# Kernel tuning notes

Measured on AMD Instinct MI355X. Metric: run time of the kernel, lower is better.

The kernel has to match this reference:

```python
import jax, jax.numpy as jnp
import numpy as np

LN_EPS = 1e-12


def setup_inputs() -> dict:
    key = jax.random.key(0)
    ks = jax.random.split(key, 10)
    B, S, W, D, H = 16, 512, 5, 200, 768
    std = 0.02
    return {
        "layer_output": jax.random.normal(ks[0], (B, S, H), dtype=jnp.float32),
        "word_embeddings": jax.random.normal(ks[1], (B, S, W, D), dtype=jnp.float32),
        "word_mask": jax.random.randint(ks[2], (B, S, W), 0, 2, dtype=jnp.int64),
        "W1": jax.random.normal(ks[3], (D, H), dtype=jnp.float32) * std,
        "b1": jnp.zeros((H,), dtype=jnp.float32),
        "W2": jax.random.normal(ks[4], (H, H), dtype=jnp.float32) * std,
        "b2": jnp.zeros((H,), dtype=jnp.float32),
        "attn_W": jax.random.normal(ks[5], (H, H), dtype=jnp.float32) * std,
        "ln_gamma": jnp.ones((H,), dtype=jnp.float32),
        "ln_beta": jnp.zeros((H,), dtype=jnp.float32),
    }


def reference(layer_output, word_embeddings, word_mask, W1, b1, W2, b2, attn_W, ln_gamma, ln_beta):
    # word_transform: Linear -> Tanh -> Linear (dropout = identity in eval)
    we = jnp.tanh(jnp.einsum("bswd,dh->bswh", word_embeddings, W1) + b1)
    we = jnp.einsum("bswh,hk->bswk", we, W2) + b2  # [B,S,W,H]

    # bilinear word attention: (x @ attn_W) . word_outputs -> score over W
    q = jnp.einsum("bsh,hk->bsk", layer_output, attn_W)  # [B,S,H]
    alpha = jnp.einsum("bsk,bswk->bsw", q, we)            # [B,S,W]
    alpha = alpha + (1.0 - word_mask.astype(alpha.dtype)) * -10000.0
    alpha = jax.nn.softmax(alpha, axis=-1)

    # weighted sum over words + residual
    agg = jnp.einsum("bsw,bswh->bsh", alpha, we)
    h = layer_output + agg

    # LayerNorm (fuse_layer; dropout = identity in eval)
    mu = jnp.mean(h, axis=-1, keepdims=True)
    var = jnp.mean(jnp.square(h - mu), axis=-1, keepdims=True)
    return (h - mu) * jax.lax.rsqrt(var + LN_EPS) * ln_gamma + ln_beta
```

## Files before the change

### kernel.cpp

```cpp
#include <hip/hip_runtime.h>
#include <hip/hip_bf16.h>
#include <math.h>


typedef __attribute__((ext_vector_type(8))) short bf16x8;
typedef __attribute__((ext_vector_type(4))) float f32x4;

__device__ __forceinline__ unsigned short f2bf_bits(float f) {
    __hip_bfloat16 h = __float2bfloat16(f);
    return *reinterpret_cast<unsigned short*>(&h);
}
__device__ __forceinline__ float bf_bits2f(unsigned short u) {
    union { unsigned int i; float f; } v; v.i = ((unsigned int)u) << 16; return v.f;
}
__device__ __forceinline__ float tanh_fast(float x) {
    float xc = fminf(fmaxf(x, -9.f), 9.f);
    float t  = __expf(2.f * xc);
    return (t - 1.f) * __builtin_amdgcn_rcpf(t + 1.f);
}
__device__ __forceinline__ bf16x8 pack8(float4 a, float4 b) {
    union { bf16x8 v; unsigned short s[8]; } u;
    u.s[0]=f2bf_bits(a.x); u.s[1]=f2bf_bits(a.y); u.s[2]=f2bf_bits(a.z); u.s[3]=f2bf_bits(a.w);
    u.s[4]=f2bf_bits(b.x); u.s[5]=f2bf_bits(b.y); u.s[6]=f2bf_bits(b.z); u.s[7]=f2bf_bits(b.w);
    return u.v;
}

__device__ __forceinline__ void async_cp16(const void* g, void* lds) {
#if __has_builtin(__builtin_amdgcn_global_load_lds)
    auto gp = (const __attribute__((address_space(1))) unsigned int*)g;
    auto lp = (__attribute__((address_space(3))) unsigned int*)lds;
    __builtin_amdgcn_global_load_lds(gp, lp, 16, 0, 0);
#else
    *(uint4*)lds = *(const uint4*)g;
#endif
}

__device__ __forceinline__ void sched_fence()  { asm volatile("" ::: "memory"); }
__device__ __forceinline__ void wait8_barrier(){ asm volatile("s_waitcnt vmcnt(8)\ns_barrier" ::: "memory"); }
__device__ __forceinline__ void wait4_barrier(){ asm volatile("s_waitcnt vmcnt(4)\ns_barrier" ::: "memory"); }
__device__ __forceinline__ void wait0_barrier(){ asm volatile("s_waitcnt vmcnt(0)\ns_barrier" ::: "memory"); }
__device__ __forceinline__ void barrier_only() { asm volatile("s_barrier" ::: "memory"); }
__device__ __forceinline__ void lgkm_barrier() { asm volatile("s_waitcnt lgkmcnt(0)\ns_barrier" ::: "memory"); }

template<bool F32SRC, bool HAS_BIAS, bool TANH_ACT, bool RESID, bool OUT_BF16,
         int N, int K, int KREAL>
__device__ __forceinline__ void gemm_body(
    const void* __restrict__ Ap, const void* __restrict__ Btp,
    const float* __restrict__ bias, const float* __restrict__ resid,
    void* __restrict__ outp, int m0, int n0, unsigned char* smem)
{
    constexpr int NIT = K / 64;
    const int tid  = threadIdx.x;
    const int lane = tid & 63;
    const int wave = tid >> 6;
    const int wm   = wave & 1;
    const int wn   = wave >> 1;
    const int row16 = lane & 15;
    const int kq    = lane >> 4;

    f32x4 acc[4][4];
#pragma unroll
    for (int i = 0; i < 4; i++)
#pragma unroll
        for (int j = 0; j < 4; j++) acc[i][j] = (f32x4){0.f, 0.f, 0.f, 0.f};

    auto compute_tile = [&](const unsigned short* As, const unsigned short* Bs, bool full) {
        bf16x8 af[2][4], bg[2][4];
#pragma unroll
        for (int mi = 0; mi < 4; mi++) {
            const int r = wm * 64 + mi * 16 + row16;
            af[0][mi] = *(const bf16x8*)&As[r * 64 + (kq ^ (r & 7)) * 8];
            if (full) af[1][mi] = *(const bf16x8*)&As[r * 64 + ((4 + kq) ^ (r & 7)) * 8];
        }
#pragma unroll
        for (int ni = 0; ni < 4; ni++) {
            const int r = wn * 64 + ni * 16 + row16;
            bg[0][ni] = *(const bf16x8*)&Bs[r * 64 + (kq ^ (r & 7)) * 8];
            if (full) bg[1][ni] = *(const bf16x8*)&Bs[r * 64 + ((4 + kq) ^ (r & 7)) * 8];
        }
        __builtin_amdgcn_s_setprio(1);
#pragma unroll
        for (int mi = 0; mi < 4; mi++)
#pragma unroll
            for (int ni = 0; ni < 4; ni++)
                acc[mi][ni] = __builtin_amdgcn_mfma_f32_16x16x32_bf16(
                    af[0][mi], bg[0][ni], acc[mi][ni], 0, 0, 0);
        if (full) {
#pragma unroll
            for (int mi = 0; mi < 4; mi++)
#pragma unroll
                for (int ni = 0; ni < 4; ni++)
                    acc[mi][ni] = __builtin_amdgcn_mfma_f32_16x16x32_bf16(
                        af[1][mi], bg[1][ni], acc[mi][ni], 0, 0, 0);
        }
        __builtin_amdgcn_s_setprio(0);
    };

    if constexpr (F32SRC) {
        const float* A32 = (const float*)Ap;
        const float* B32 = (const float*)Btp;
        unsigned short* As = (unsigned short*)smem;
        unsigned short* Bs = As + 8192;
        for (int t = 0; t < NIT; ++t) {
#pragma unroll
            for (int i = 0; i < 4; ++i) {
                const int c = i * 256 + tid;
                const int row = c >> 3, sl = c & 7;
                const int kcc = sl ^ (row & 7);
                const float* sa = A32 + (size_t)(m0 + row) * K + t * 64 + kcc * 8;
                *(bf16x8*)&As[row * 64 + sl * 8] = pack8(*(const float4*)sa, *(const float4*)(sa + 4));
                const float* sb = B32 + (size_t)(n0 + row) * K + t * 64 + kcc * 8;
                *(bf16x8*)&Bs[row * 64 + sl * 8] = pack8(*(const float4*)sb, *(const float4*)(sb + 4));
            }
            __syncthreads();
            compute_tile(As, Bs, true);
            __syncthreads();
        }
    } else {
        const __hip_bfloat16* A  = (const __hip_bfloat16*)Ap;
        const __hip_bfloat16* Bt = (const __hip_bfloat16*)Btp;
        const int rsub = lane >> 3;
        const int slot = lane & 7;
        const int kc   = slot ^ rsub;
        const __hip_bfloat16* gA = A  + (size_t)(m0 + wave * 32 + rsub) * K + kc * 8;
        const __hip_bfloat16* gB = Bt + (size_t)(n0 + wave * 32 + rsub) * K + kc * 8;
        unsigned short* lA0 = (unsigned short*)smem + wave * 2048 + lane * 8;
        unsigned short* lB0 = lA0 + 8192;

        auto stage = [&](int t, int buf) {
            unsigned short* lA = lA0 + buf * 16384;
            unsigned short* lB = lB0 + buf * 16384;
            const __hip_bfloat16* a = gA + t * 64;
            const __hip_bfloat16* b = gB + t * 64;
#pragma unroll
            for (int i = 0; i < 4; i++) {
                async_cp16(a + (size_t)(8 * i) * K, lA + i * 512);
                async_cp16(b + (size_t)(8 * i) * K, lB + i * 512);
            }
            sched_fence();
        };

        stage(0, 0);
        if (NIT > 1) stage(1, 1);
#pragma unroll
        for (int t = 0; t < NIT; ++t) {
            if (t == NIT - 1) wait0_barrier(); else wait8_barrier();
            const unsigned short* As = (const unsigned short*)(smem + (t & 1) * 32768);
            const unsigned short* Bs = As + 8192;
            compute_tile(As, Bs, (t * 64 + 32 < KREAL));
            barrier_only();
            if (t + 2 < NIT) stage(t + 2, t & 1);
        }
    }

    if (OUT_BF16) {
        unsigned short* rep = (unsigned short*)smem;
#pragma unroll
        for (int ni = 0; ni < 4; ni++) {
            const int c = wn * 64 + ni * 16 + row16;
            float bcol = HAS_BIAS ? bias[n0 + c] : 0.f;
#pragma unroll
            for (int mi = 0; mi < 4; mi++)
#pragma unroll
                for (int r = 0; r < 4; r++) {
                    const int rr = wm * 64 + mi * 16 + kq * 4 + r;
                    float v = acc[mi][ni][r];
                    if (HAS_BIAS) v += bcol;
                    if (TANH_ACT) v = tanh_fast(v);
                    rep[rr * 132 + c] = f2bf_bits(v);
                }
        }
        __syncthreads();
#pragma unroll
        for (int p = 0; p < 8; p++) {
            const int lin = p * 256 + tid;
            const int row = lin >> 4;
            const int c8  = lin & 15;
            const unsigned short* s = &rep[row * 132 + c8 * 8];
            union { uint4 u; unsigned long long q[2]; } d;
            d.q[0] = *(const unsigned long long*)(s);
            d.q[1] = *(const unsigned long long*)(s + 4);
            *(uint4*)((__hip_bfloat16*)outp + (size_t)(m0 + row) * N + n0 + c8 * 8) = d.u;
        }
    } else {
        float* rep = (float*)smem;
#pragma unroll
        for (int h = 0; h < 2; h++) {
            if (wm == h) {
#pragma unroll
                for (int ni = 0; ni < 4; ni++) {
                    const int c = wn * 64 + ni * 16 + row16;
                    float bcol = HAS_BIAS ? bias[n0 + c] : 0.f;
#pragma unroll
                    for (int mi = 0; mi < 4; mi++)
#pragma unroll
                        for (int r = 0; r < 4; r++) {
                            const int rr = mi * 16 + kq * 4 + r;
                            float v = acc[mi][ni][r];
                            if (HAS_BIAS) v += bcol;
                            if (TANH_ACT) v = tanh_fast(v);
                            rep[rr * 132 + c] = v;
                        }
                }
            }
            __syncthreads();
#pragma unroll
            for (int p = 0; p < 8; p++) {
                const int lin = p * 256 + tid;
                const int row = lin >> 5;
                const int c4  = lin & 31;
                float4 v = *(const float4*)&rep[row * 132 + c4 * 4];
                const int grow = m0 + h * 64 + row;
                if (RESID) {
                    float4 rv = *(const float4*)&resid[(size_t)grow * N + n0 + c4 * 4];
                    v.x += rv.x; v.y += rv.y; v.z += rv.z; v.w += rv.w;
                }
                *(float4*)((float*)outp + (size_t)grow * N + n0 + c4 * 4) = v;
            }
            __syncthreads();
        }
    }
}

template<bool HAS_BIAS, bool TANH_ACT, bool RESID, bool OUT_BF16, int N, int K, int GX>
__global__ __launch_bounds__(256) void mfma_gemm(
    const __hip_bfloat16* __restrict__ A,
    const __hip_bfloat16* __restrict__ Bt,
    const float* __restrict__ bias,
    const float* __restrict__ resid,
    void* __restrict__ outp)
{
    __shared__ __align__(16) unsigned char smem[65536];
    int bx, by;
    {
        const int total = gridDim.x;
        const int per_xcd = total >> 3;
        if ((total & 7) == 0 && (per_xcd % GX) == 0) {
            int xcd = blockIdx.x & 7, idx = blockIdx.x >> 3;
            int lin = xcd * per_xcd + idx;
            by = lin / GX; bx = lin % GX;
        } else { by = blockIdx.x / GX; bx = blockIdx.x % GX; }
    }
    gemm_body<false, HAS_BIAS, TANH_ACT, RESID, OUT_BF16, N, K, K>(
        A, Bt, bias, resid, outp, by * 128, bx * 128, smem);
}

__global__ __launch_bounds__(256) void tgemm_kernel(
    const __hip_bfloat16* __restrict__ Eb,
    const __hip_bfloat16* __restrict__ W1Tb,
    const float* __restrict__ b1,
    __hip_bfloat16* __restrict__ Tb)
{
    __shared__ __align__(16) unsigned char smem[132096];
    unsigned short* Bs_all = (unsigned short*)smem;
    unsigned short* As_all = (unsigned short*)(smem + 65536);
    unsigned short* rep    = (unsigned short*)(smem + 98304);

    const int tid  = threadIdx.x;
    const int lane = tid & 63;
    const int wave = tid >> 6;
    const int wm   = wave & 1;
    const int wn   = wave >> 1;
    const int row16 = lane & 15;
    const int kq    = lane >> 4;

    const int lin = (blockIdx.x & 7) * 48 + (blockIdx.x >> 3);
    const int mg  = lin / 6;
    const int bx  = lin % 6;

#pragma unroll
    for (int kt = 0; kt < 4; ++kt)
#pragma unroll
        for (int i = 0; i < 4; ++i) {
            const int c = i * 256 + tid;
            const int row = c >> 3, sl = c & 7;
            const int kcc = sl ^ (row & 7);
            async_cp16(W1Tb + (size_t)(bx * 128 + row) * 256 + kt * 64 + kcc * 8,
                       Bs_all + kt * 8192 + c * 8);
        }
    sched_fence();

    auto stageA = [&](int mt, int t, int buf) {
        const int m0 = mg * 640 + mt * 128;
#pragma unroll
        for (int i = 0; i < 4; ++i) {
            const int c = i * 256 + tid;
            const int row = c >> 3, sl = c & 7;
            const int kcc = sl ^ (row & 7);
            async_cp16(Eb + (size_t)(m0 + row) * 256 + t * 64 + kcc * 8,
                       As_all + buf * 8192 + c * 8);
        }
        sched_fence();
    };

    stageA(0, 0, 0);
    stageA(0, 1, 1);

    for (int mt = 0; mt < 5; ++mt) {
        f32x4 acc[4][4];
#pragma unroll
        for (int i = 0; i < 4; i++)
#pragma unroll
            for (int j = 0; j < 4; j++) acc[i][j] = (f32x4){0.f, 0.f, 0.f, 0.f};

#pragma unroll
        for (int t = 0; t < 4; ++t) {
            const int idx = mt * 4 + t;
            if (idx == 19) wait0_barrier(); else wait4_barrier();

            const unsigned short* As = As_all + (idx & 1) * 8192;
            const unsigned short* Bs = Bs_all + t * 8192;
            const bool full = (t < 3);

            bf16x8 af[2][4], bg[2][4];
#pragma unroll
            for (int mi = 0; mi < 4; mi++) {
                const int r = wm * 64 + mi * 16 + row16;
                af[0][mi] = *(const bf16x8*)&As[r * 64 + (kq ^ (r & 7)) * 8];
                if (full) af[1][mi] = *(const bf16x8*)&As[r * 64 + ((4 + kq) ^ (r & 7)) * 8];
            }
#pragma unroll
            for (int ni = 0; ni < 4; ni++) {
                const int r = wn * 64 + ni * 16 + row16;
                bg[0][ni] = *(const bf16x8*)&Bs[r * 64 + (kq ^ (r & 7)) * 8];
                if (full) bg[1][ni] = *(const bf16x8*)&Bs[r * 64 + ((4 + kq) ^ (r & 7)) * 8];
            }
            __builtin_amdgcn_s_setprio(1);
#pragma unroll
            for (int mi = 0; mi < 4; mi++)
#pragma unroll
                for (int ni = 0; ni < 4; ni++)
                    acc[mi][ni] = __builtin_amdgcn_mfma_f32_16x16x32_bf16(
                        af[0][mi], bg[0][ni], acc[mi][ni], 0, 0, 0);
            if (full) {
#pragma unroll
                for (int mi = 0; mi < 4; mi++)
#pragma unroll
                    for (int ni = 0; ni < 4; ni++)
                        acc[mi][ni] = __builtin_amdgcn_mfma_f32_16x16x32_bf16(
                            af[1][mi], bg[1][ni], acc[mi][ni], 0, 0, 0);
            }
            __builtin_amdgcn_s_setprio(0);
            barrier_only();
            if (idx + 2 < 20) stageA((idx + 2) >> 2, (idx + 2) & 3, idx & 1);
        }

        const int m0 = mg * 640 + mt * 128;
#pragma unroll
        for (int ni = 0; ni < 4; ni++) {
            const int c = wn * 64 + ni * 16 + row16;
            const float bcol = b1[bx * 128 + c];
#pragma unroll
            for (int mi = 0; mi < 4; mi++)
#pragma unroll
                for (int r = 0; r < 4; r++) {
                    const int rr = wm * 64 + mi * 16 + kq * 4 + r;
                    rep[rr * 132 + c] = f2bf_bits(tanh_fast(acc[mi][ni][r] + bcol));
                }
        }
        lgkm_barrier();
#pragma unroll
        for (int p = 0; p < 8; p++) {
            const int linc = p * 256 + tid;
            const int row = linc >> 4;
            const int c8  = linc & 15;
            const unsigned short* s = &rep[row * 132 + c8 * 8];
            union { uint4 u; unsigned long long q[2]; } d;
            d.q[0] = *(const unsigned long long*)(s);
            d.q[1] = *(const unsigned long long*)(s + 4);
            *(uint4*)(Tb + (size_t)(m0 + row) * 768 + bx * 128 + c8 * 8) = d.u;
        }
        if (mt < 4) barrier_only();
    }
}

__global__ __launch_bounds__(256) void prep_kernel(
    const float* __restrict__ x,  __hip_bfloat16* __restrict__ xb,
    const float* __restrict__ w2,
    const float* __restrict__ aw,
    const float* __restrict__ E,  __hip_bfloat16* __restrict__ Eb,
    const float* __restrict__ W1, __hip_bfloat16* __restrict__ W1Tb,
    __hip_bfloat16* __restrict__ W2Tb,
    __hip_bfloat16* __restrict__ Ctb)
{
    __shared__ __align__(16) unsigned char smem[33792];
    float (*tile)[33] = (float(*)[33])smem;
    const int b = blockIdx.x, tid = threadIdx.x;
    if (b < 36) {
        gemm_body<true, false, false, false, true, 768, 768, 768>(
            w2, aw, nullptr, nullptr, Ctb, (b / 6) * 128, (b % 6) * 128, smem);
    } else if (b < 804) {
        const float* in; __hip_bfloat16* outb; int R, C, Rpad, t;
        if (b < 228) { t = b - 36;  in = W1; outb = W1Tb; R = 200; C = 768; Rpad = 256; }
        else         { t = b - 228; in = w2; outb = W2Tb; R = 768; C = 768; Rpad = 768; }
        const int c0 = (t % 24) * 32, r0 = (t / 24) * 32;
        const int xx = tid & 31, yy = tid >> 5;
#pragma unroll
        for (int i = 0; i < 32; i += 8) {
            int r = r0 + yy + i;
            tile[yy + i][xx] = (r < R) ? in[(size_t)r * C + c0 + xx] : 0.f;
        }
        __syncthreads();
#pragma unroll
        for (int i = 0; i < 32; i += 8)
            outb[(size_t)(c0 + yy + i) * Rpad + r0 + xx] = __float2bfloat16(tile[xx][yy + i]);
    } else if (b < 1572) {
        const long long base = (long long)(b - 804) * 2048 + tid;
        float4 v[8];
#pragma unroll
        for (int j = 0; j < 8; j++) v[j] = ((const float4*)x)[base + j * 256];
#pragma unroll
        for (int j = 0; j < 8; j++)
            ((ushort4*)xb)[base + j * 256] =
                make_ushort4(f2bf_bits(v[j].x), f2bf_bits(v[j].y), f2bf_bits(v[j].z), f2bf_bits(v[j].w));
    } else {
        const int lane = tid & 63, wave = tid >> 6;
        const long long r0 = (long long)(b - 1572) * 32 + wave * 8;
        const int k = lane * 4;
        float4 v[8];
#pragma unroll
        for (int j = 0; j < 8; j++) {
            v[j] = make_float4(0.f, 0.f, 0.f, 0.f);
            if (k < 200) v[j] = *(const float4*)&E[(r0 + j) * 200 + k];
        }
#pragma unroll
        for (int j = 0; j < 8; j++)
            *(ushort4*)&Eb[(r0 + j) * 256 + k] =
                make_ushort4(f2bf_bits(v[j].x), f2bf_bits(v[j].y), f2bf_bits(v[j].z), f2bf_bits(v[j].w));
    }
}

__global__ __launch_bounds__(256) void attn_kernel(
    const __hip_bfloat16* __restrict__ T,
    const __hip_bfloat16* P,
    const int* __restrict__ mask,
    __hip_bfloat16* S)
{
    const int lane = threadIdx.x & 63;
    const int wave = threadIdx.x >> 6;
    const int r    = blockIdx.x * 4 + wave;
    const int base = lane * 12;

    float pv[12];
    {
        const ushort4* pp = (const ushort4*)((const unsigned short*)P + (size_t)r * 768 + base);
        ushort4 u0 = pp[0], u1 = pp[1], u2 = pp[2];
        unsigned short us[12] = {u0.x,u0.y,u0.z,u0.w, u1.x,u1.y,u1.z,u1.w, u2.x,u2.y,u2.z,u2.w};
#pragma unroll
        for (int j = 0; j < 12; j++) pv[j] = bf_bits2f(us[j]);
    }
    float tv[5][12], part[5];
#pragma unroll
    for (int w = 0; w < 5; w++) {
        const ushort4* tp = (const ushort4*)((const unsigned short*)T + ((size_t)r * 5 + w) * 768 + base);
        ushort4 u0 = tp[0], u1 = tp[1], u2 = tp[2];
        unsigned short us[12] = {u0.x,u0.y,u0.z,u0.w, u1.x,u1.y,u1.z,u1.w, u2.x,u2.y,u2.z,u2.w};
        float s = 0.f;
#pragma unroll
        for (int j = 0; j < 12; j++) { tv[w][j] = bf_bits2f(us[j]); s += tv[w][j] * pv[j]; }
        part[w] = s;
    }
#pragma unroll
    for (int off = 32; off > 0; off >>= 1)
#pragma unroll
        for (int w = 0; w < 5; w++)
            part[w] += __shfl_xor(part[w], off, 64);

    float logit[5], mx = -1e30f;
#pragma unroll
    for (int w = 0; w < 5; w++) {
        float m = (float)mask[(size_t)r * 5 + w];
        logit[w] = part[w] - 10000.0f * (1.0f - m);
        mx = fmaxf(mx, logit[w]);
    }
    float se = 0.f;
#pragma unroll
    for (int w = 0; w < 5; w++) { logit[w] = expf(logit[w] - mx); se += logit[w]; }
    const float inv = 1.0f / se;

    unsigned short os[12];
#pragma unroll
    for (int j = 0; j < 12; j++) {
        float s = 0.f;
#pragma unroll
        for (int w = 0; w < 5; w++) s += logit[w] * tv[w][j];
        os[j] = f2bf_bits(s * inv);
    }
    ushort4* sp = (ushort4*)((unsigned short*)S + (size_t)r * 768 + base);
    sp[0] = make_ushort4(os[0], os[1], os[2],  os[3]);
    sp[1] = make_ushort4(os[4], os[5], os[6],  os[7]);
    sp[2] = make_ushort4(os[8], os[9], os[10], os[11]);
}

__global__ __launch_bounds__(256) void ln_kernel(
    const float* __restrict__ Hbuf, const float* __restrict__ gamma,
    const float* __restrict__ beta, float* __restrict__ out)
{
    const int lane = threadIdx.x & 63;
    const int wave = threadIdx.x >> 6;
    const int r    = blockIdx.x * 4 + wave;
    const float* hr = Hbuf + (size_t)r * 768 + lane * 12;

    float v[12];
    {
        float4 a = *(const float4*)(hr);
        float4 b = *(const float4*)(hr + 4);
        float4 c = *(const float4*)(hr + 8);
        v[0]=a.x; v[1]=a.y; v[2]=a.z; v[3]=a.w;
        v[4]=b.x; v[5]=b.y; v[6]=b.z; v[7]=b.w;
        v[8]=c.x; v[9]=c.y; v[10]=c.z; v[11]=c.w;
    }
    float s = 0.f;
#pragma unroll
    for (int j = 0; j < 12; j++) s += v[j];
#pragma unroll
    for (int off = 32; off > 0; off >>= 1) s += __shfl_xor(s, off, 64);
    const float mu = s * (1.f / 768.f);
    float vs = 0.f;
#pragma unroll
    for (int j = 0; j < 12; j++) { float d = v[j] - mu; vs += d * d; }
#pragma unroll
    for (int off = 32; off > 0; off >>= 1) vs += __shfl_xor(vs, off, 64);
    const float rs = rsqrtf(vs * (1.f / 768.f) + 1e-12f);

    float o[12];
#pragma unroll
    for (int j = 0; j < 12; j++) {
        int h = lane * 12 + j;
        o[j] = (v[j] - mu) * rs * gamma[h] + beta[h];
    }
    float* orow = out + (size_t)r * 768 + lane * 12;
    *(float4*)(orow)     = make_float4(o[0], o[1], o[2],  o[3]);
    *(float4*)(orow + 4) = make_float4(o[4], o[5], o[6],  o[7]);
    *(float4*)(orow + 8) = make_float4(o[8], o[9], o[10], o[11]);
}

extern "C" void kernel_launch(void* const* d_in, const int* in_sizes, int n_in,
                              void* d_out, int out_size, void* d_ws, size_t ws_size,
                              hipStream_t stream)
{
    const float* x      = (const float*)d_in[0];
    const float* E      = (const float*)d_in[1];
    const int*   mask   = (const int*)d_in[2];
    const float* W1     = (const float*)d_in[3];
    const float* b1     = (const float*)d_in[4];
    const float* W2     = (const float*)d_in[5];
    const float* b2     = (const float*)d_in[6];
    const float* attn_W = (const float*)d_in[7];
    const float* gamma  = (const float*)d_in[8];
    const float* beta   = (const float*)d_in[9];
    float* out = (float*)d_out;

    const int BS = 8192, H = 768, M1 = 40960, KP = 256;

    char* p = (char*)d_ws;
    auto alloc = [&](size_t bytes) { char* q = p; p += (bytes + 255) & ~(size_t)255; return q; };
    __hip_bfloat16* xb    = (__hip_bfloat16*)alloc((size_t)BS * H * 2);
    __hip_bfloat16* W2Tb  = (__hip_bfloat16*)alloc((size_t)H * H * 2);
    __hip_bfloat16* Ctb   = (__hip_bfloat16*)alloc((size_t)H * H * 2);
    __hip_bfloat16* W1Tb  = (__hip_bfloat16*)alloc((size_t)H * KP * 2);
    __hip_bfloat16* Tb    = (__hip_bfloat16*)alloc((size_t)M1 * H * 2);
    __hip_bfloat16* Eb    = (__hip_bfloat16*)alloc((size_t)M1 * KP * 2);
    float* Hb = (float*)Tb;
    __hip_bfloat16* Pb = Eb;
    __hip_bfloat16* Sb = Pb;

    prep_kernel<<<2852, 256, 0, stream>>>(x, xb, W2, attn_W, E, Eb, W1, W1Tb, W2Tb, Ctb);

    tgemm_kernel<<<384, 256, 0, stream>>>(Eb, W1Tb, b1, Tb);

    mfma_gemm<false, false, false, true, 768, 768, 6><<<384, 256, 0, stream>>>(
        xb, Ctb, nullptr, nullptr, Pb);

    attn_kernel<<<BS / 4, 256, 0, stream>>>(Tb, Pb, mask, Sb);

    mfma_gemm<true, false, true, false, 768, 768, 6><<<384, 256, 0, stream>>>(
        Sb, W2Tb, b2, x, Hb);

    ln_kernel<<<BS / 4, 256, 0, stream>>>(Hb, gamma, beta, out);
}
```

Before: 244.5 us.

## Restructure tanh GEMM to keep A tile resident and loop over N tiles

The first GEMM kernel (E·W1 + tanh) now gives each block one 128-row A tile held in LDS for the whole K range and loops over all six 128-column N tiles, reloading W1 per tile. Previously each block held one W1 column tile and streamed five A tiles through double buffers. The block grows to 512 threads (8 waves, 2 M-fragments each) on a 320-block grid. The aim is to read E once and spread the work over more waves. The cost is that the W1 load is no longer overlapped with compute (a full wait before each N tile), LDS use grows, and the epilogue is split into two halves with extra barriers.

```diff
diff --git a/kernel.cpp b/kernel.cpp
--- a/kernel.cpp
+++ b/kernel.cpp
@@ -37,7 +37,6 @@
 
 __device__ __forceinline__ void sched_fence()  { asm volatile("" ::: "memory"); }
 __device__ __forceinline__ void wait8_barrier(){ asm volatile("s_waitcnt vmcnt(8)\ns_barrier" ::: "memory"); }
-__device__ __forceinline__ void wait4_barrier(){ asm volatile("s_waitcnt vmcnt(4)\ns_barrier" ::: "memory"); }
 __device__ __forceinline__ void wait0_barrier(){ asm volatile("s_waitcnt vmcnt(0)\ns_barrier" ::: "memory"); }
 __device__ __forceinline__ void barrier_only() { asm volatile("s_barrier" ::: "memory"); }
 __device__ __forceinline__ void lgkm_barrier() { asm volatile("s_waitcnt lgkmcnt(0)\ns_barrier" ::: "memory"); }
@@ -245,77 +244,70 @@
         A, Bt, bias, resid, outp, by * 128, bx * 128, smem);
 }
 
-__global__ __launch_bounds__(256) void tgemm_kernel(
+__global__ __launch_bounds__(512) void tgemm_kernel(
     const __hip_bfloat16* __restrict__ Eb,
     const __hip_bfloat16* __restrict__ W1Tb,
     const float* __restrict__ b1,
     __hip_bfloat16* __restrict__ Tb)
 {
-    __shared__ __align__(16) unsigned char smem[132096];
-    unsigned short* Bs_all = (unsigned short*)smem;
-    unsigned short* As_all = (unsigned short*)(smem + 65536);
-    unsigned short* rep    = (unsigned short*)(smem + 98304);
+    __shared__ __align__(16) unsigned char smem[148480];
+    unsigned short* Aall = (unsigned short*)smem;
+    unsigned short* Ball = (unsigned short*)(smem + 65536);
+    unsigned short* rep  = (unsigned short*)(smem + 131072);
 
     const int tid  = threadIdx.x;
     const int lane = tid & 63;
     const int wave = tid >> 6;
-    const int wm   = wave & 1;
-    const int wn   = wave >> 1;
+    const int wm   = wave & 3;
+    const int wn   = wave >> 2;
     const int row16 = lane & 15;
     const int kq    = lane >> 4;
 
-    const int lin = (blockIdx.x & 7) * 48 + (blockIdx.x >> 3);
-    const int mg  = lin / 6;
-    const int bx  = lin % 6;
+    const int blk = (blockIdx.x & 7) * 40 + (blockIdx.x >> 3);
+    const int m0  = blk * 128;
 
 #pragma unroll
     for (int kt = 0; kt < 4; ++kt)
 #pragma unroll
-        for (int i = 0; i < 4; ++i) {
-            const int c = i * 256 + tid;
+        for (int i = 0; i < 2; ++i) {
+            const int c = i * 512 + tid;
             const int row = c >> 3, sl = c & 7;
             const int kcc = sl ^ (row & 7);
-            async_cp16(W1Tb + (size_t)(bx * 128 + row) * 256 + kt * 64 + kcc * 8,
-                       Bs_all + kt * 8192 + c * 8);
+            async_cp16(Eb + (size_t)(m0 + row) * 256 + kt * 64 + kcc * 8,
+                       Aall + kt * 8192 + c * 8);
         }
     sched_fence();
 
-    auto stageA = [&](int mt, int t, int buf) {
-        const int m0 = mg * 640 + mt * 128;
-#pragma unroll
-        for (int i = 0; i < 4; ++i) {
-            const int c = i * 256 + tid;
-            const int row = c >> 3, sl = c & 7;
-            const int kcc = sl ^ (row & 7);
-            async_cp16(Eb + (size_t)(m0 + row) * 256 + t * 64 + kcc * 8,
-                       As_all + buf * 8192 + c * 8);
-        }
+    for (int nt = 0; nt < 6; ++nt) {
+#pragma unroll
+        for (int kt = 0; kt < 4; ++kt)
+#pragma unroll
+            for (int i = 0; i < 2; ++i) {
+                const int c = i * 512 + tid;
+                const int row = c >> 3, sl = c & 7;
+                const int kcc = sl ^ (row & 7);
+                async_cp16(W1Tb + (size_t)(nt * 128 + row) * 256 + kt * 64 + kcc * 8,
+                           Ball + kt * 8192 + c * 8);
+            }
         sched_fence();
-    };
-
-    stageA(0, 0, 0);
-    stageA(0, 1, 1);
-
-    for (int mt = 0; mt < 5; ++mt) {
-        f32x4 acc[4][4];
-#pragma unroll
-        for (int i = 0; i < 4; i++)
+        wait0_barrier();
+
+        f32x4 acc[2][4];
+#pragma unroll
+        for (int i = 0; i < 2; i++)
 #pragma unroll
             for (int j = 0; j < 4; j++) acc[i][j] = (f32x4){0.f, 0.f, 0.f, 0.f};
 
 #pragma unroll
-        for (int t = 0; t < 4; ++t) {
-            const int idx = mt * 4 + t;
-            if (idx == 19) wait0_barrier(); else wait4_barrier();
-
-            const unsigned short* As = As_all + (idx & 1) * 8192;
-            const unsigned short* Bs = Bs_all + t * 8192;
-            const bool full = (t < 3);
-
-            bf16x8 af[2][4], bg[2][4];
-#pragma unroll
-            for (int mi = 0; mi < 4; mi++) {
-                const int r = wm * 64 + mi * 16 + row16;
+        for (int kt = 0; kt < 4; ++kt) {
+            const unsigned short* As = Aall + kt * 8192;
+            const unsigned short* Bs = Ball + kt * 8192;
+            const bool full = (kt < 3);
+
+            bf16x8 af[2][2], bg[2][4];
+#pragma unroll
+            for (int mi = 0; mi < 2; mi++) {
+                const int r = wm * 32 + mi * 16 + row16;
                 af[0][mi] = *(const bf16x8*)&As[r * 64 + (kq ^ (r & 7)) * 8];
                 if (full) af[1][mi] = *(const bf16x8*)&As[r * 64 + ((4 + kq) ^ (r & 7)) * 8];
             }
@@ -327,50 +319,53 @@
             }
             __builtin_amdgcn_s_setprio(1);
 #pragma unroll
-            for (int mi = 0; mi < 4; mi++)
+            for (int mi = 0; mi < 2; mi++)
 #pragma unroll
                 for (int ni = 0; ni < 4; ni++)
                     acc[mi][ni] = __builtin_amdgcn_mfma_f32_16x16x32_bf16(
                         af[0][mi], bg[0][ni], acc[mi][ni], 0, 0, 0);
             if (full) {
 #pragma unroll
-                for (int mi = 0; mi < 4; mi++)
+                for (int mi = 0; mi < 2; mi++)
 #pragma unroll
                     for (int ni = 0; ni < 4; ni++)
                         acc[mi][ni] = __builtin_amdgcn_mfma_f32_16x16x32_bf16(
                             af[1][mi], bg[1][ni], acc[mi][ni], 0, 0, 0);
             }
             __builtin_amdgcn_s_setprio(0);
+        }
+        barrier_only();
+
+#pragma unroll
+        for (int h = 0; h < 2; ++h) {
+            if ((wm >> 1) == h) {
+#pragma unroll
+                for (int ni = 0; ni < 4; ni++) {
+                    const int c = wn * 64 + ni * 16 + row16;
+                    const float bcol = b1[nt * 128 + c];
+#pragma unroll
+                    for (int mi = 0; mi < 2; mi++)
+#pragma unroll
+                        for (int r = 0; r < 4; r++) {
+                            const int rr = (wm & 1) * 32 + mi * 16 + kq * 4 + r;
+                            rep[rr * 132 + c] = f2bf_bits(tanh_fast(acc[mi][ni][r] + bcol));
+                        }
+                }
+            }
+            lgkm_barrier();
+#pragma unroll
+            for (int p = 0; p < 2; p++) {
+                const int lin = p * 512 + tid;
+                const int row = lin >> 4;
+                const int c8  = lin & 15;
+                const unsigned short* s = &rep[row * 132 + c8 * 8];
+                union { uint4 u; unsigned long long q[2]; } d;
+                d.q[0] = *(const unsigned long long*)(s);
+                d.q[1] = *(const unsigned long long*)(s + 4);
+                *(uint4*)(Tb + (size_t)(m0 + h * 64 + row) * 768 + nt * 128 + c8 * 8) = d.u;
+            }
             barrier_only();
-            if (idx + 2 < 20) stageA((idx + 2) >> 2, (idx + 2) & 3, idx & 1);
-        }
-
-        const int m0 = mg * 640 + mt * 128;
-#pragma unroll
-        for (int ni = 0; ni < 4; ni++) {
-            const int c = wn * 64 + ni * 16 + row16;
-            const float bcol = b1[bx * 128 + c];
-#pragma unroll
-            for (int mi = 0; mi < 4; mi++)
-#pragma unroll
-                for (int r = 0; r < 4; r++) {
-                    const int rr = wm * 64 + mi * 16 + kq * 4 + r;
-                    rep[rr * 132 + c] = f2bf_bits(tanh_fast(acc[mi][ni][r] + bcol));
-                }
-        }
-        lgkm_barrier();
-#pragma unroll
-        for (int p = 0; p < 8; p++) {
-            const int linc = p * 256 + tid;
-            const int row = linc >> 4;
-            const int c8  = linc & 15;
-            const unsigned short* s = &rep[row * 132 + c8 * 8];
-            union { uint4 u; unsigned long long q[2]; } d;
-            d.q[0] = *(const unsigned long long*)(s);
-            d.q[1] = *(const unsigned long long*)(s + 4);
-            *(uint4*)(Tb + (size_t)(m0 + row) * 768 + bx * 128 + c8 * 8) = d.u;
-        }
-        if (mt < 4) barrier_only();
+        }
     }
 }
 
@@ -567,7 +562,7 @@
 
     prep_kernel<<<2852, 256, 0, stream>>>(x, xb, W2, attn_W, E, Eb, W1, W1Tb, W2Tb, Ctb);
 
-    tgemm_kernel<<<384, 256, 0, stream>>>(Eb, W1Tb, b1, Tb);
+    tgemm_kernel<<<320, 512, 0, stream>>>(Eb, W1Tb, b1, Tb);
 
     mfma_gemm<false, false, false, true, 768, 768, 6><<<384, 256, 0, stream>>>(
         xb, Ctb, nullptr, nullptr, Pb);
```

New measurement: 267.7 us. +9.5%, slower.
